# Kernel tuning notes

Hardware: AMD Instinct MI355X
Metric: run time of the kernel (lower is better)

## Reference

```python
import jax, jax.numpy as jnp
import numpy as np

PROCESSING_STEPS = 3


def setup_inputs() -> dict:
    key = jax.random.key(0)
    ks = jax.random.split(key, 8)
    B, N, d = 1024, 128, 128
    y = jax.random.normal(ks[0], (B, N, d), dtype=jnp.float32)
    lengths = jax.random.randint(ks[1], (B,), 1, N + 1, dtype=jnp.int32)
    s = 0.05
    W_ih = jax.random.normal(ks[2], (4 * d, 2 * d), dtype=jnp.float32) * s
    W_hh = jax.random.normal(ks[3], (4 * d, d), dtype=jnp.float32) * s
    b_ih = jax.random.normal(ks[4], (4 * d,), dtype=jnp.float32) * s
    b_hh = jax.random.normal(ks[5], (4 * d,), dtype=jnp.float32) * s
    W_m = jax.random.normal(ks[6], (1, 2 * d), dtype=jnp.float32) * s
    b_m = jax.random.normal(ks[7], (1,), dtype=jnp.float32) * s
    mean = jnp.zeros((1,), jnp.float32)
    stddev = jnp.ones((1,), jnp.float32)
    return {"y": y, "lengths": lengths, "W_ih": W_ih, "W_hh": W_hh,
            "b_ih": b_ih, "b_hh": b_hh, "W_m": W_m, "b_m": b_m,
            "mean": mean, "stddev": stddev}


def reference(y, lengths, W_ih, W_hh, b_ih, b_hh, W_m, b_m, mean, stddev):
    # y: [B, N, d] padded atomwise representation; lengths: valid atoms per molecule
    B, N, d = y.shape
    mask = jnp.arange(N)[None, :] < lengths[:, None]          # [B, N]
    maskf = mask.astype(y.dtype)[..., None]                    # [B, N, 1]
    neg_inf = jnp.finfo(y.dtype).min

    q_star = jnp.zeros((B, 2 * d), y.dtype)
    h = jnp.zeros((B, d), y.dtype)
    c = jnp.zeros((B, d), y.dtype)

    def step(carry, _):
        q_star, h, c = carry
        # single-layer LSTM cell (PyTorch gate order i, f, g, o)
        gates = q_star @ W_ih.T + b_ih + h @ W_hh.T + b_hh     # [B, 4d]
        i, f, g, o = jnp.split(gates, 4, axis=-1)
        c2 = jax.nn.sigmoid(f) * c + jax.nn.sigmoid(i) * jnp.tanh(g)
        h2 = jax.nn.sigmoid(o) * jnp.tanh(c2)
        q = h2                                                  # [B, d]
        # attention: gather q per atom, segment softmax, scatter_add
        e = jnp.einsum('bnd,bd->bn', y, q)                      # [B, N]
        e = jnp.where(mask, e, neg_inf)
        a = jax.nn.softmax(e, axis=-1)[..., None] * maskf       # [B, N, 1]
        r = jnp.sum(a * y, axis=1)                              # [B, d]
        return (jnp.concatenate([q, r], axis=-1), h2, c2), None

    (q_star, h, c), _ = jax.lax.scan(step, (q_star, h, c), None,
                                     length=PROCESSING_STEPS)
    out = q_star @ W_m.T + b_m                                  # [B, 1]
    return out * stddev + mean
```

## Files before the change

### kernel.cpp

```cpp
#include <hip/hip_runtime.h>
#include <math.h>

#define BB 1024
#define NN 128
#define DD 128
#define GG 512

__device__ __forceinline__ float sigmoidf_(float x) { return 1.0f / (1.0f + expf(-x)); }

__global__ __launch_bounds__(256) void k_prep(
    const float* __restrict__ W_ih, const float* __restrict__ W_hh,
    const float* __restrict__ b_ih, const float* __restrict__ b_hh,
    float* __restrict__ Wc, float* __restrict__ biasv, float* __restrict__ gbase,
    float* __restrict__ h1, float* __restrict__ c1) {
  int b = blockIdx.x, t = threadIdx.x;
  if (b < 64) {
    int base = b * 1024;
    for (int i = t; i < 1024; i += 256) {
      int idx = base + i;
      int j = idx >> 7, d = idx & 127;
      Wc[idx] = W_ih[(j << 8) + d] + W_hh[idx];
    }
  } else {
    __shared__ float bv[GG];
    __shared__ float h1l[DD];
    for (int j = t; j < GG; j += 256) bv[j] = b_ih[j] + b_hh[j];
    __syncthreads();
    if (t < DD) {
      float cc = sigmoidf_(bv[t]) * tanhf(bv[256 + t]);
      float hh = sigmoidf_(bv[384 + t]) * tanhf(cc);
      h1l[t] = hh;
      if (b == 64) { c1[t] = cc; h1[t] = hh; }
    }
    if (b == 64) for (int j = t; j < GG; j += 256) biasv[j] = bv[j];
    __syncthreads();
    int j0 = (b - 64) * 128;
    if (t < 128) {
      int j = j0 + t;
      float acc = bv[j];
      const float* wi = W_ih + (j << 8);
      const float* wh = W_hh + (j << 7);
      #pragma unroll 8
      for (int d = 0; d < DD; ++d) acc = fmaf(wi[d] + wh[d], h1l[d], acc);
      gbase[j] = acc;
    }
  }
}

__global__ __launch_bounds__(256) void k_attn(
    const float* __restrict__ y, const int* __restrict__ lengths,
    const float* __restrict__ qsrc, int q_bcast,
    float* __restrict__ rN,
    const float* __restrict__ Wm, const float* __restrict__ bm,
    const float* __restrict__ mn, const float* __restrict__ sd,
    float* __restrict__ out, int is_final) {
  __shared__ float ql[DD];
  __shared__ float rp[4][DD];
  __shared__ float redm[4], reds[4], redf[4];

  int t = threadIdx.x, lane = t & 63, w = t >> 6;
  int sub = lane & 15, g = lane >> 4;
  int m = blockIdx.x;
  int len = lengths[m];
  const float* yb = y + (size_t)m * (NN * DD);
  int d0 = sub << 3;

  if (t < DD) ql[t] = q_bcast ? qsrc[t] : qsrc[m * DD + t];
  __syncthreads();

  float4 q0 = *(const float4*)&ql[d0];
  float4 q1 = *(const float4*)&ql[d0 + 4];

  float4 va[8], vb[8];
  float ee[8];
  int wbase = w << 2;

  #pragma unroll
  for (int it = 0; it < 8; ++it) {
    int nw = (it << 4) + wbase;
    if (nw < len) {
      int n = nw + g;
      int nc = (n < len) ? n : (len - 1);
      const float4* yr = (const float4*)(yb + nc * DD + d0);
      va[it] = yr[0];
      vb[it] = yr[1];
      float p = fmaf(va[it].x, q0.x, fmaf(va[it].y, q0.y,
                fmaf(va[it].z, q0.z, fmaf(va[it].w, q0.w,
                fmaf(vb[it].x, q1.x, fmaf(vb[it].y, q1.y,
                fmaf(vb[it].z, q1.z, vb[it].w * q1.w)))))));
      #pragma unroll
      for (int s = 1; s < 16; s <<= 1) p += __shfl_xor(p, s, 64);
      ee[it] = (n < len) ? p : -3.0e38f;
    } else {
      ee[it] = -3.0e38f;
    }
  }

  float mloc = ee[0];
  #pragma unroll
  for (int it = 1; it < 8; ++it) mloc = fmaxf(mloc, ee[it]);
  #pragma unroll
  for (int s = 1; s < 64; s <<= 1) mloc = fmaxf(mloc, __shfl_xor(mloc, s, 64));

  float a[8];
  float sl = 0.0f;
  #pragma unroll
  for (int it = 0; it < 8; ++it) { a[it] = expf(ee[it] - mloc); sl += a[it]; }
  #pragma unroll
  for (int s = 1; s < 64; s <<= 1) sl += __shfl_xor(sl, s, 64);
  if (lane == 0) { redm[w] = mloc; reds[w] = sl; }
  __syncthreads();

  float m0_ = redm[0], m1_ = redm[1], m2_ = redm[2], m3_ = redm[3];
  float mx = fmaxf(fmaxf(m0_, m1_), fmaxf(m2_, m3_));
  float Zraw = reds[0] * expf(m0_ - mx) + reds[1] * expf(m1_ - mx) +
               reds[2] * expf(m2_ - mx) + reds[3] * expf(m3_ - mx);
  float wscale = expf(mloc - mx) * (16.0f / Zraw);

  float4 r0 = {0.f, 0.f, 0.f, 0.f}, r1 = {0.f, 0.f, 0.f, 0.f};
  #pragma unroll
  for (int it = 0; it < 8; ++it) {
    int nw = (it << 4) + wbase;
    if (nw < len) {
      float av = a[it];
      r0.x = fmaf(av, va[it].x, r0.x); r0.y = fmaf(av, va[it].y, r0.y);
      r0.z = fmaf(av, va[it].z, r0.z); r0.w = fmaf(av, va[it].w, r0.w);
      r1.x = fmaf(av, vb[it].x, r1.x); r1.y = fmaf(av, vb[it].y, r1.y);
      r1.z = fmaf(av, vb[it].z, r1.z); r1.w = fmaf(av, vb[it].w, r1.w);
    }
  }
  r0.x *= wscale; r0.y *= wscale; r0.z *= wscale; r0.w *= wscale;
  r1.x *= wscale; r1.y *= wscale; r1.z *= wscale; r1.w *= wscale;

  #pragma unroll
  for (int s = 16; s < 64; s <<= 1) {
    r0.x += __shfl_xor(r0.x, s, 64); r0.y += __shfl_xor(r0.y, s, 64);
    r0.z += __shfl_xor(r0.z, s, 64); r0.w += __shfl_xor(r0.w, s, 64);
    r1.x += __shfl_xor(r1.x, s, 64); r1.y += __shfl_xor(r1.y, s, 64);
    r1.z += __shfl_xor(r1.z, s, 64); r1.w += __shfl_xor(r1.w, s, 64);
  }
  if (g == 0) {
    *(float4*)&rp[w][d0] = r0;
    *(float4*)&rp[w][d0 + 4] = r1;
  }
  __syncthreads();

  float r_ = 0.0f;
  if (t < DD) {
    r_ = rp[0][t] + rp[1][t] + rp[2][t] + rp[3][t];
    if (!is_final) rN[m * DD + t] = r_;
  }
  if (is_final) {
    float part = (t < DD) ? (Wm[t] * ql[t] + Wm[DD + t] * r_) : 0.0f;
    #pragma unroll
    for (int s = 1; s < 64; s <<= 1) part += __shfl_xor(part, s, 64);
    if (lane == 0) redf[w] = part;
    __syncthreads();
    if (t == 0) out[m] = (redf[0] + redf[1] + redf[2] + redf[3] + bm[0]) * sd[0] + mn[0];
  }
}

__global__ __launch_bounds__(512) void k_lstm(
    const float* __restrict__ W_ih, const float* __restrict__ Wc,
    const float* __restrict__ gb,
    const float* __restrict__ h_inN,
    const float* __restrict__ c_in, int c_bcast,
    const float* __restrict__ rNin,
    float* __restrict__ h_outN, float* __restrict__ c_outT) {
  __shared__ float xl[64 * 129];
  __shared__ float ht[64 * 9];
  int t = threadIdx.x;
  int ml = t & 63, wid = t >> 6;
  int m0 = blockIdx.x << 6;
  int m = m0 + ml;
  int jb = __builtin_amdgcn_readfirstlane((blockIdx.y << 3) + wid);

  float ai = gb[jb], af = gb[DD + jb], ag = gb[2 * DD + jb], ao = gb[3 * DD + jb];

  if (h_inN) {
    #pragma unroll
    for (int k = 0; k < 16; ++k) {
      int i = (k << 9) + t;
      int mm = i >> 7, dd = i & 127;
      xl[mm * 129 + dd] = h_inN[(m0 + mm) * DD + dd];
    }
    __syncthreads();
    const float* w0 = Wc + jb * DD;
    const float* w1 = Wc + (128 + jb) * DD;
    const float* w2 = Wc + (256 + jb) * DD;
    const float* w3 = Wc + (384 + jb) * DD;
    #pragma unroll 8
    for (int d = 0; d < DD; ++d) {
      float xd = xl[ml * 129 + d];
      ai = fmaf(w0[d], xd, ai); af = fmaf(w1[d], xd, af);
      ag = fmaf(w2[d], xd, ag); ao = fmaf(w3[d], xd, ao);
    }
    __syncthreads();
  }

  #pragma unroll
  for (int k = 0; k < 16; ++k) {
    int i = (k << 9) + t;
    int mm = i >> 7, dd = i & 127;
    xl[mm * 129 + dd] = rNin[(m0 + mm) * DD + dd];
  }
  __syncthreads();
  {
    const float* w0 = W_ih + jb * 256 + 128;
    const float* w1 = W_ih + (128 + jb) * 256 + 128;
    const float* w2 = W_ih + (256 + jb) * 256 + 128;
    const float* w3 = W_ih + (384 + jb) * 256 + 128;
    #pragma unroll 8
    for (int d = 0; d < DD; ++d) {
      float xd = xl[ml * 129 + d];
      ai = fmaf(w0[d], xd, ai); af = fmaf(w1[d], xd, af);
      ag = fmaf(w2[d], xd, ag); ao = fmaf(w3[d], xd, ao);
    }
  }

  float cin = c_bcast ? c_in[jb] : c_in[jb * BB + m];
  float cc = fmaf(sigmoidf_(af), cin, sigmoidf_(ai) * tanhf(ag));
  float hh = sigmoidf_(ao) * tanhf(cc);
  ht[ml * 9 + wid] = hh;
  if (c_outT) c_outT[jb * BB + m] = cc;
  __syncthreads();
  {
    int jj = t & 7, mm = t >> 3;
    h_outN[(m0 + mm) * DD + (blockIdx.y << 3) + jj] = ht[mm * 9 + jj];
  }
}

extern "C" void kernel_launch(void* const* d_in, const int* in_sizes, int n_in,
                              void* d_out, int out_size, void* d_ws, size_t ws_size,
                              hipStream_t stream) {
  const float* y    = (const float*)d_in[0];
  const int*   len  = (const int*)  d_in[1];
  const float* W_ih = (const float*)d_in[2];
  const float* W_hh = (const float*)d_in[3];
  const float* b_ih = (const float*)d_in[4];
  const float* b_hh = (const float*)d_in[5];
  const float* W_m  = (const float*)d_in[6];
  const float* b_m  = (const float*)d_in[7];
  const float* mean = (const float*)d_in[8];
  const float* sd   = (const float*)d_in[9];
  float* out = (float*)d_out;

  float* ws = (float*)d_ws;
  float* Wc    = ws;
  float* biasv = ws + 65536;
  float* gbase = ws + 66048;
  float* h1    = ws + 66560;
  float* c1    = ws + 66688;
  float* rN    = ws + 66816;
  float* h2N   = ws + 197888;
  float* c2T   = ws + 328960;
  float* h3N   = ws + 460032;

  k_prep<<<68, 256, 0, stream>>>(W_ih, W_hh, b_ih, b_hh, Wc, biasv, gbase, h1, c1);

  k_attn<<<BB, 256, 0, stream>>>(y, len, h1, 1, rN, W_m, b_m, mean, sd, nullptr, 0);
  k_lstm<<<dim3(16, 16), 512, 0, stream>>>(W_ih, Wc, gbase, nullptr, c1, 1, rN, h2N, c2T);
  k_attn<<<BB, 256, 0, stream>>>(y, len, h2N, 0, rN, W_m, b_m, mean, sd, nullptr, 0);
  k_lstm<<<dim3(16, 16), 512, 0, stream>>>(W_ih, Wc, biasv, h2N, c2T, 0, rN, h3N, nullptr);
  k_attn<<<BB, 256, 0, stream>>>(y, len, h3N, 0, nullptr, W_m, b_m, mean, sd, out, 1);
}
```

Baseline: 63.62 us.

## Fold prep kernel into attention and LSTM kernels, pair molecules per block

Removes the separate k_prep launch. The first attention pass now computes the initial h from the biases inline, and the first LSTM step builds the combined W_ih+W_hh matrix and the base gates in-kernel. The attention kernel now handles two molecules per 512-thread block, pairing m with 1023-m to balance variable lengths, and issues all y loads before the dot products to raise memory-level parallelism. The cost is redundant bias and weight work repeated in every LSTM block, plus extra registers from loading all rows unconditionally, including clamped rows past the valid length.

```diff
diff --git a/kernel.cpp b/kernel.cpp
--- a/kernel.cpp
+++ b/kernel.cpp
@@ -4,86 +4,63 @@
 #define BB 1024
 #define NN 128
 #define DD 128
-#define GG 512
 
 __device__ __forceinline__ float sigmoidf_(float x) { return 1.0f / (1.0f + expf(-x)); }
 
-__global__ __launch_bounds__(256) void k_prep(
-    const float* __restrict__ W_ih, const float* __restrict__ W_hh,
+__global__ __launch_bounds__(512) void k_attn(
+    const float* __restrict__ y, const int* __restrict__ lengths,
+    const float* __restrict__ qsrc,
     const float* __restrict__ b_ih, const float* __restrict__ b_hh,
-    float* __restrict__ Wc, float* __restrict__ biasv, float* __restrict__ gbase,
-    float* __restrict__ h1, float* __restrict__ c1) {
-  int b = blockIdx.x, t = threadIdx.x;
-  if (b < 64) {
-    int base = b * 1024;
-    for (int i = t; i < 1024; i += 256) {
-      int idx = base + i;
-      int j = idx >> 7, d = idx & 127;
-      Wc[idx] = W_ih[(j << 8) + d] + W_hh[idx];
-    }
-  } else {
-    __shared__ float bv[GG];
-    __shared__ float h1l[DD];
-    for (int j = t; j < GG; j += 256) bv[j] = b_ih[j] + b_hh[j];
-    __syncthreads();
-    if (t < DD) {
-      float cc = sigmoidf_(bv[t]) * tanhf(bv[256 + t]);
-      float hh = sigmoidf_(bv[384 + t]) * tanhf(cc);
-      h1l[t] = hh;
-      if (b == 64) { c1[t] = cc; h1[t] = hh; }
-    }
-    if (b == 64) for (int j = t; j < GG; j += 256) biasv[j] = bv[j];
-    __syncthreads();
-    int j0 = (b - 64) * 128;
-    if (t < 128) {
-      int j = j0 + t;
-      float acc = bv[j];
-      const float* wi = W_ih + (j << 8);
-      const float* wh = W_hh + (j << 7);
-      #pragma unroll 8
-      for (int d = 0; d < DD; ++d) acc = fmaf(wi[d] + wh[d], h1l[d], acc);
-      gbase[j] = acc;
-    }
-  }
-}
-
-__global__ __launch_bounds__(256) void k_attn(
-    const float* __restrict__ y, const int* __restrict__ lengths,
-    const float* __restrict__ qsrc, int q_bcast,
     float* __restrict__ rN,
     const float* __restrict__ Wm, const float* __restrict__ bm,
     const float* __restrict__ mn, const float* __restrict__ sd,
     float* __restrict__ out, int is_final) {
-  __shared__ float ql[DD];
-  __shared__ float rp[4][DD];
-  __shared__ float redm[4], reds[4], redf[4];
+  __shared__ float ql[2][DD];
+  __shared__ float rp[2][4][DD];
+  __shared__ float redm[2][4], reds[2][4], redf[2][4];
 
   int t = threadIdx.x, lane = t & 63, w = t >> 6;
+  int h = w >> 2, w4 = w & 3;
   int sub = lane & 15, g = lane >> 4;
-  int m = blockIdx.x;
+  int m = h ? (1023 - (int)blockIdx.x) : (int)blockIdx.x;
   int len = lengths[m];
   const float* yb = y + (size_t)m * (NN * DD);
   int d0 = sub << 3;
-
-  if (t < DD) ql[t] = q_bcast ? qsrc[t] : qsrc[m * DD + t];
-  __syncthreads();
-
-  float4 q0 = *(const float4*)&ql[d0];
-  float4 q1 = *(const float4*)&ql[d0 + 4];
+  int th = t & 255;
+
+  if (th < DD) {
+    if (qsrc) {
+      ql[h][th] = qsrc[m * DD + th];
+    } else {
+      float bv0 = b_ih[th] + b_hh[th];
+      float bvg = b_ih[256 + th] + b_hh[256 + th];
+      float bvo = b_ih[384 + th] + b_hh[384 + th];
+      float cc = sigmoidf_(bv0) * tanhf(bvg);
+      ql[h][th] = sigmoidf_(bvo) * tanhf(cc);
+    }
+  }
+  __syncthreads();
+
+  float4 q0 = *(const float4*)&ql[h][d0];
+  float4 q1 = *(const float4*)&ql[h][d0 + 4];
 
   float4 va[8], vb[8];
+  int wbase = w4 << 2;
+  #pragma unroll
+  for (int it = 0; it < 8; ++it) {
+    int n = (it << 4) + wbase + g;
+    int nc = (n < len) ? n : (len - 1);
+    const float4* yr = (const float4*)(yb + nc * DD + d0);
+    va[it] = yr[0];
+    vb[it] = yr[1];
+  }
+
   float ee[8];
-  int wbase = w << 2;
-
   #pragma unroll
   for (int it = 0; it < 8; ++it) {
     int nw = (it << 4) + wbase;
     if (nw < len) {
       int n = nw + g;
-      int nc = (n < len) ? n : (len - 1);
-      const float4* yr = (const float4*)(yb + nc * DD + d0);
-      va[it] = yr[0];
-      vb[it] = yr[1];
       float p = fmaf(va[it].x, q0.x, fmaf(va[it].y, q0.y,
                 fmaf(va[it].z, q0.z, fmaf(va[it].w, q0.w,
                 fmaf(vb[it].x, q1.x, fmaf(vb[it].y, q1.y,
@@ -108,13 +85,13 @@
   for (int it = 0; it < 8; ++it) { a[it] = expf(ee[it] - mloc); sl += a[it]; }
   #pragma unroll
   for (int s = 1; s < 64; s <<= 1) sl += __shfl_xor(sl, s, 64);
-  if (lane == 0) { redm[w] = mloc; reds[w] = sl; }
-  __syncthreads();
-
-  float m0_ = redm[0], m1_ = redm[1], m2_ = redm[2], m3_ = redm[3];
+  if (lane == 0) { redm[h][w4] = mloc; reds[h][w4] = sl; }
+  __syncthreads();
+
+  float m0_ = redm[h][0], m1_ = redm[h][1], m2_ = redm[h][2], m3_ = redm[h][3];
   float mx = fmaxf(fmaxf(m0_, m1_), fmaxf(m2_, m3_));
-  float Zraw = reds[0] * expf(m0_ - mx) + reds[1] * expf(m1_ - mx) +
-               reds[2] * expf(m2_ - mx) + reds[3] * expf(m3_ - mx);
+  float Zraw = reds[h][0] * expf(m0_ - mx) + reds[h][1] * expf(m1_ - mx) +
+               reds[h][2] * expf(m2_ - mx) + reds[h][3] * expf(m3_ - mx);
   float wscale = expf(mloc - mx) * (16.0f / Zraw);
 
   float4 r0 = {0.f, 0.f, 0.f, 0.f}, r1 = {0.f, 0.f, 0.f, 0.f};
@@ -140,44 +117,79 @@
     r1.z += __shfl_xor(r1.z, s, 64); r1.w += __shfl_xor(r1.w, s, 64);
   }
   if (g == 0) {
-    *(float4*)&rp[w][d0] = r0;
-    *(float4*)&rp[w][d0 + 4] = r1;
+    *(float4*)&rp[h][w4][d0] = r0;
+    *(float4*)&rp[h][w4][d0 + 4] = r1;
   }
   __syncthreads();
 
   float r_ = 0.0f;
-  if (t < DD) {
-    r_ = rp[0][t] + rp[1][t] + rp[2][t] + rp[3][t];
-    if (!is_final) rN[m * DD + t] = r_;
+  if (th < DD) {
+    r_ = rp[h][0][th] + rp[h][1][th] + rp[h][2][th] + rp[h][3][th];
+    if (!is_final) rN[m * DD + th] = r_;
   }
   if (is_final) {
-    float part = (t < DD) ? (Wm[t] * ql[t] + Wm[DD + t] * r_) : 0.0f;
+    float part = (th < DD) ? (Wm[th] * ql[h][th] + Wm[DD + th] * r_) : 0.0f;
     #pragma unroll
     for (int s = 1; s < 64; s <<= 1) part += __shfl_xor(part, s, 64);
-    if (lane == 0) redf[w] = part;
-    __syncthreads();
-    if (t == 0) out[m] = (redf[0] + redf[1] + redf[2] + redf[3] + bm[0]) * sd[0] + mn[0];
+    if (lane == 0) redf[h][w4] = part;
+    __syncthreads();
+    if (th == 0)
+      out[m] = (redf[h][0] + redf[h][1] + redf[h][2] + redf[h][3] + bm[0]) * sd[0] + mn[0];
   }
 }
 
 __global__ __launch_bounds__(512) void k_lstm(
-    const float* __restrict__ W_ih, const float* __restrict__ Wc,
-    const float* __restrict__ gb,
+    const float* __restrict__ W_ih, const float* __restrict__ W_hh,
+    const float* __restrict__ b_ih, const float* __restrict__ b_hh,
+    float* __restrict__ Wc,
     const float* __restrict__ h_inN,
-    const float* __restrict__ c_in, int c_bcast,
+    const float* __restrict__ cT,
     const float* __restrict__ rNin,
-    float* __restrict__ h_outN, float* __restrict__ c_outT) {
+    float* __restrict__ h_outN, float* __restrict__ c_outT, int step) {
   __shared__ float xl[64 * 129];
+  __shared__ float h1l[DD];
   __shared__ float ht[64 * 9];
-  int t = threadIdx.x;
-  int ml = t & 63, wid = t >> 6;
-  int m0 = blockIdx.x << 6;
-  int m = m0 + ml;
-  int jb = __builtin_amdgcn_readfirstlane((blockIdx.y << 3) + wid);
-
-  float ai = gb[jb], af = gb[DD + jb], ag = gb[2 * DD + jb], ao = gb[3 * DD + jb];
-
-  if (h_inN) {
+  int t = threadIdx.x, lane = t & 63, wid = t >> 6;
+  int m0 = (int)blockIdx.x << 6, m = m0 + lane;
+  int jb = __builtin_amdgcn_readfirstlane(((int)blockIdx.y << 3) + wid);
+
+  float ai, af, ag, ao, cin;
+
+  if (step == 1) {
+    if (t < DD) {
+      float bv0 = b_ih[t] + b_hh[t];
+      float bvg = b_ih[256 + t] + b_hh[256 + t];
+      float bvo = b_ih[384 + t] + b_hh[384 + t];
+      float cc = sigmoidf_(bv0) * tanhf(bvg);
+      h1l[t] = sigmoidf_(bvo) * tanhf(cc);
+    }
+    __syncthreads();
+    int d = lane << 1;
+    float acc4[4];
+    #pragma unroll
+    for (int gi = 0; gi < 4; ++gi) {
+      int j = jb + (gi << 7);
+      float2 wih = *(const float2*)&W_ih[j * 256 + d];
+      float2 whh = *(const float2*)&W_hh[(j << 7) + d];
+      float s0 = wih.x + whh.x, s1 = wih.y + whh.y;
+      if (blockIdx.x == 0) {
+        Wc[(j << 7) + d] = s0;
+        Wc[(j << 7) + d + 1] = s1;
+      }
+      float part = fmaf(s0, h1l[d], s1 * h1l[d + 1]);
+      #pragma unroll
+      for (int s = 1; s < 64; s <<= 1) part += __shfl_xor(part, s, 64);
+      acc4[gi] = part + b_ih[j] + b_hh[j];
+    }
+    ai = acc4[0]; af = acc4[1]; ag = acc4[2]; ao = acc4[3];
+    cin = sigmoidf_(b_ih[jb] + b_hh[jb]) *
+          tanhf(b_ih[256 + jb] + b_hh[256 + jb]);
+  } else {
+    ai = b_ih[jb] + b_hh[jb];
+    af = b_ih[128 + jb] + b_hh[128 + jb];
+    ag = b_ih[256 + jb] + b_hh[256 + jb];
+    ao = b_ih[384 + jb] + b_hh[384 + jb];
+    cin = cT[(jb << 10) + m];
     #pragma unroll
     for (int k = 0; k < 16; ++k) {
       int i = (k << 9) + t;
@@ -185,15 +197,15 @@
       xl[mm * 129 + dd] = h_inN[(m0 + mm) * DD + dd];
     }
     __syncthreads();
-    const float* w0 = Wc + jb * DD;
-    const float* w1 = Wc + (128 + jb) * DD;
-    const float* w2 = Wc + (256 + jb) * DD;
-    const float* w3 = Wc + (384 + jb) * DD;
+    const float* w0 = Wc + (jb << 7);
+    const float* w1 = Wc + ((128 + jb) << 7);
+    const float* w2 = Wc + ((256 + jb) << 7);
+    const float* w3 = Wc + ((384 + jb) << 7);
     #pragma unroll 8
-    for (int d = 0; d < DD; ++d) {
-      float xd = xl[ml * 129 + d];
-      ai = fmaf(w0[d], xd, ai); af = fmaf(w1[d], xd, af);
-      ag = fmaf(w2[d], xd, ag); ao = fmaf(w3[d], xd, ao);
+    for (int dd = 0; dd < DD; ++dd) {
+      float xd = xl[lane * 129 + dd];
+      ai = fmaf(w0[dd], xd, ai); af = fmaf(w1[dd], xd, af);
+      ag = fmaf(w2[dd], xd, ag); ao = fmaf(w3[dd], xd, ao);
     }
     __syncthreads();
   }
@@ -211,22 +223,21 @@
     const float* w2 = W_ih + (256 + jb) * 256 + 128;
     const float* w3 = W_ih + (384 + jb) * 256 + 128;
     #pragma unroll 8
-    for (int d = 0; d < DD; ++d) {
-      float xd = xl[ml * 129 + d];
-      ai = fmaf(w0[d], xd, ai); af = fmaf(w1[d], xd, af);
-      ag = fmaf(w2[d], xd, ag); ao = fmaf(w3[d], xd, ao);
-    }
-  }
-
-  float cin = c_bcast ? c_in[jb] : c_in[jb * BB + m];
+    for (int dd = 0; dd < DD; ++dd) {
+      float xd = xl[lane * 129 + dd];
+      ai = fmaf(w0[dd], xd, ai); af = fmaf(w1[dd], xd, af);
+      ag = fmaf(w2[dd], xd, ag); ao = fmaf(w3[dd], xd, ao);
+    }
+  }
+
   float cc = fmaf(sigmoidf_(af), cin, sigmoidf_(ai) * tanhf(ag));
   float hh = sigmoidf_(ao) * tanhf(cc);
-  ht[ml * 9 + wid] = hh;
-  if (c_outT) c_outT[jb * BB + m] = cc;
+  ht[lane * 9 + wid] = hh;
+  if (c_outT) c_outT[(jb << 10) + m] = cc;
   __syncthreads();
   {
     int jj = t & 7, mm = t >> 3;
-    h_outN[(m0 + mm) * DD + (blockIdx.y << 3) + jj] = ht[mm * 9 + jj];
+    h_outN[(m0 + mm) * DD + ((int)blockIdx.y << 3) + jj] = ht[mm * 9 + jj];
   }
 }
 
@@ -246,21 +257,20 @@
   float* out = (float*)d_out;
 
   float* ws = (float*)d_ws;
-  float* Wc    = ws;
-  float* biasv = ws + 65536;
-  float* gbase = ws + 66048;
-  float* h1    = ws + 66560;
-  float* c1    = ws + 66688;
-  float* rN    = ws + 66816;
-  float* h2N   = ws + 197888;
-  float* c2T   = ws + 328960;
-  float* h3N   = ws + 460032;
-
-  k_prep<<<68, 256, 0, stream>>>(W_ih, W_hh, b_ih, b_hh, Wc, biasv, gbase, h1, c1);
-
-  k_attn<<<BB, 256, 0, stream>>>(y, len, h1, 1, rN, W_m, b_m, mean, sd, nullptr, 0);
-  k_lstm<<<dim3(16, 16), 512, 0, stream>>>(W_ih, Wc, gbase, nullptr, c1, 1, rN, h2N, c2T);
-  k_attn<<<BB, 256, 0, stream>>>(y, len, h2N, 0, rN, W_m, b_m, mean, sd, nullptr, 0);
-  k_lstm<<<dim3(16, 16), 512, 0, stream>>>(W_ih, Wc, biasv, h2N, c2T, 0, rN, h3N, nullptr);
-  k_attn<<<BB, 256, 0, stream>>>(y, len, h3N, 0, nullptr, W_m, b_m, mean, sd, out, 1);
+  float* Wc  = ws;
+  float* rN  = ws + 65536;
+  float* h2N = ws + 196608;
+  float* c2T = ws + 327680;
+  float* h3N = ws + 458752;
+
+  k_attn<<<512, 512, 0, stream>>>(y, len, nullptr, b_ih, b_hh, rN,
+                                  W_m, b_m, mean, sd, nullptr, 0);
+  k_lstm<<<dim3(16, 16), 512, 0, stream>>>(W_ih, W_hh, b_ih, b_hh, Wc,
+                                           nullptr, nullptr, rN, h2N, c2T, 1);
+  k_attn<<<512, 512, 0, stream>>>(y, len, h2N, b_ih, b_hh, rN,
+                                  W_m, b_m, mean, sd, nullptr, 0);
+  k_lstm<<<dim3(16, 16), 512, 0, stream>>>(W_ih, W_hh, b_ih, b_hh, Wc,
+                                           h2N, c2T, rN, h3N, nullptr, 2);
+  k_attn<<<512, 512, 0, stream>>>(y, len, h3N, b_ih, b_hh, nullptr,
+                                  W_m, b_m, mean, sd, out, 1);
 }
```

New measurement: 61.35 us. -3.6%, faster.

## Fuse all attention and LSTM steps into one persistent per-molecule-pair kernel

Applied to the files above, without the earlier changes.

Replaces the three attention launches and two LSTM launches with a single kernel in which each 512-thread block handles two molecules (one per half). Each molecule's y rows are kept in registers and reused across all three processing steps, and the LSTM gates are computed in-block from a combined weight matrix. This removes repeated reads of y from global memory, the intermediate h/r/c round-trips and four kernel launches. In exchange every block re-reads the full 512x256 weight matrix from L2/global, and register pressure under launch_bounds(512,4) may limit occupancy.

```diff
diff --git a/kernel.cpp b/kernel.cpp
--- a/kernel.cpp
+++ b/kernel.cpp
@@ -4,230 +4,247 @@
 #define BB 1024
 #define NN 128
 #define DD 128
-#define GG 512
 
 __device__ __forceinline__ float sigmoidf_(float x) { return 1.0f / (1.0f + expf(-x)); }
 
-__global__ __launch_bounds__(256) void k_prep(
+__global__ __launch_bounds__(256) void k_prep2(
     const float* __restrict__ W_ih, const float* __restrict__ W_hh,
     const float* __restrict__ b_ih, const float* __restrict__ b_hh,
-    float* __restrict__ Wc, float* __restrict__ biasv, float* __restrict__ gbase,
-    float* __restrict__ h1, float* __restrict__ c1) {
+    float* __restrict__ Wfull, float* __restrict__ gbase) {
   int b = blockIdx.x, t = threadIdx.x;
   if (b < 64) {
-    int base = b * 1024;
-    for (int i = t; i < 1024; i += 256) {
+    int base = b * 2048;
+    for (int i = t; i < 2048; i += 256) {
       int idx = base + i;
-      int j = idx >> 7, d = idx & 127;
-      Wc[idx] = W_ih[(j << 8) + d] + W_hh[idx];
+      int j = idx >> 8, d = idx & 255;
+      float v = W_ih[(j << 8) + d];
+      if (d < 128) v += W_hh[(j << 7) + d];
+      Wfull[idx] = v;
     }
   } else {
-    __shared__ float bv[GG];
     __shared__ float h1l[DD];
-    for (int j = t; j < GG; j += 256) bv[j] = b_ih[j] + b_hh[j];
-    __syncthreads();
     if (t < DD) {
-      float cc = sigmoidf_(bv[t]) * tanhf(bv[256 + t]);
-      float hh = sigmoidf_(bv[384 + t]) * tanhf(cc);
-      h1l[t] = hh;
-      if (b == 64) { c1[t] = cc; h1[t] = hh; }
-    }
-    if (b == 64) for (int j = t; j < GG; j += 256) biasv[j] = bv[j];
+      float bi = b_ih[t] + b_hh[t];
+      float bg = b_ih[256 + t] + b_hh[256 + t];
+      float bo = b_ih[384 + t] + b_hh[384 + t];
+      float cc = sigmoidf_(bi) * tanhf(bg);
+      h1l[t] = sigmoidf_(bo) * tanhf(cc);
+    }
     __syncthreads();
     int j0 = (b - 64) * 128;
     if (t < 128) {
       int j = j0 + t;
-      float acc = bv[j];
-      const float* wi = W_ih + (j << 8);
-      const float* wh = W_hh + (j << 7);
+      float acc = b_ih[j] + b_hh[j];
       #pragma unroll 8
-      for (int d = 0; d < DD; ++d) acc = fmaf(wi[d] + wh[d], h1l[d], acc);
+      for (int d = 0; d < DD; ++d)
+        acc = fmaf(W_ih[(j << 8) + d] + W_hh[(j << 7) + d], h1l[d], acc);
       gbase[j] = acc;
     }
   }
 }
 
-__global__ __launch_bounds__(256) void k_attn(
+struct SMX {
+  float ql[2][DD];
+  float c1l[DD];
+  float rp[2][4][DD];
+  float xcat[2][256];
+  float g2[2][512];
+  float c2l[2][DD];
+  float redm[2][4], reds[2][4], redf[2][4];
+};
+
+__global__ __launch_bounds__(512, 4) void k_fused(
     const float* __restrict__ y, const int* __restrict__ lengths,
-    const float* __restrict__ qsrc, int q_bcast,
-    float* __restrict__ rN,
+    const float* __restrict__ Wfull, const float* __restrict__ gbase,
+    const float* __restrict__ b_ih, const float* __restrict__ b_hh,
     const float* __restrict__ Wm, const float* __restrict__ bm,
     const float* __restrict__ mn, const float* __restrict__ sd,
-    float* __restrict__ out, int is_final) {
-  __shared__ float ql[DD];
-  __shared__ float rp[4][DD];
-  __shared__ float redm[4], reds[4], redf[4];
-
-  int t = threadIdx.x, lane = t & 63, w = t >> 6;
-  int sub = lane & 15, g = lane >> 4;
-  int m = blockIdx.x;
-  int len = lengths[m];
+    float* __restrict__ out) {
+  __shared__ SMX s;
+  const int t = threadIdx.x;
+  const int lane = t & 63;
+  const int h = t >> 8;
+  const int th = t & 255;
+  const int w4 = (t >> 6) & 3;
+  const int sub = lane & 15, g = lane >> 4;
+  const int d0 = sub << 3;
+  const int wbase = w4 << 2;
+  const int m = h ? (1023 - (int)blockIdx.x) : (int)blockIdx.x;
+  const int len = lengths[m];
   const float* yb = y + (size_t)m * (NN * DD);
-  int d0 = sub << 3;
-
-  if (t < DD) ql[t] = q_bcast ? qsrc[t] : qsrc[m * DD + t];
-  __syncthreads();
-
-  float4 q0 = *(const float4*)&ql[d0];
-  float4 q1 = *(const float4*)&ql[d0 + 4];
+
+  if (th < DD) {
+    float bi = b_ih[th] + b_hh[th];
+    float bg = b_ih[256 + th] + b_hh[256 + th];
+    float bo = b_ih[384 + th] + b_hh[384 + th];
+    float cc = sigmoidf_(bi) * tanhf(bg);
+    s.ql[h][th] = sigmoidf_(bo) * tanhf(cc);
+    if (h == 0) s.c1l[th] = cc;
+  }
 
   float4 va[8], vb[8];
-  float ee[8];
-  int wbase = w << 2;
-
   #pragma unroll
   for (int it = 0; it < 8; ++it) {
-    int nw = (it << 4) + wbase;
-    if (nw < len) {
-      int n = nw + g;
-      int nc = (n < len) ? n : (len - 1);
-      const float4* yr = (const float4*)(yb + nc * DD + d0);
-      va[it] = yr[0];
-      vb[it] = yr[1];
-      float p = fmaf(va[it].x, q0.x, fmaf(va[it].y, q0.y,
-                fmaf(va[it].z, q0.z, fmaf(va[it].w, q0.w,
-                fmaf(vb[it].x, q1.x, fmaf(vb[it].y, q1.y,
-                fmaf(vb[it].z, q1.z, vb[it].w * q1.w)))))));
+    int n = (it << 4) + wbase + g;
+    int nc = (n < len) ? n : (len - 1);
+    const float4* yr = (const float4*)(yb + nc * DD + d0);
+    va[it] = yr[0];
+    vb[it] = yr[1];
+  }
+  __syncthreads();
+
+  auto attn = [&](float* rdst, bool is_final) {
+    float4 q0 = *(const float4*)&s.ql[h][d0];
+    float4 q1 = *(const float4*)&s.ql[h][d0 + 4];
+    float ee[8];
+    #pragma unroll
+    for (int it = 0; it < 8; ++it) {
+      int nw = (it << 4) + wbase;
+      if (nw < len) {
+        int n = nw + g;
+        float p = fmaf(va[it].x, q0.x, fmaf(va[it].y, q0.y,
+                  fmaf(va[it].z, q0.z, fmaf(va[it].w, q0.w,
+                  fmaf(vb[it].x, q1.x, fmaf(vb[it].y, q1.y,
+                  fmaf(vb[it].z, q1.z, vb[it].w * q1.w)))))));
+        #pragma unroll
+        for (int sh = 1; sh < 16; sh <<= 1) p += __shfl_xor(p, sh, 64);
+        ee[it] = (n < len) ? p : -3.0e38f;
+      } else {
+        ee[it] = -3.0e38f;
+      }
+    }
+    float mloc = ee[0];
+    #pragma unroll
+    for (int it = 1; it < 8; ++it) mloc = fmaxf(mloc, ee[it]);
+    #pragma unroll
+    for (int sh = 1; sh < 64; sh <<= 1) mloc = fmaxf(mloc, __shfl_xor(mloc, sh, 64));
+    float a[8], sl = 0.0f;
+    #pragma unroll
+    for (int it = 0; it < 8; ++it) { a[it] = expf(ee[it] - mloc); sl += a[it]; }
+    #pragma unroll
+    for (int sh = 1; sh < 64; sh <<= 1) sl += __shfl_xor(sl, sh, 64);
+    if (lane == 0) { s.redm[h][w4] = mloc; s.reds[h][w4] = sl; }
+    __syncthreads();
+    float m0_ = s.redm[h][0], m1_ = s.redm[h][1], m2_ = s.redm[h][2], m3_ = s.redm[h][3];
+    float mx = fmaxf(fmaxf(m0_, m1_), fmaxf(m2_, m3_));
+    float Zraw = s.reds[h][0] * expf(m0_ - mx) + s.reds[h][1] * expf(m1_ - mx) +
+                 s.reds[h][2] * expf(m2_ - mx) + s.reds[h][3] * expf(m3_ - mx);
+    float wscale = expf(mloc - mx) * (16.0f / Zraw);
+
+    float4 r0 = {0.f, 0.f, 0.f, 0.f}, r1 = {0.f, 0.f, 0.f, 0.f};
+    #pragma unroll
+    for (int it = 0; it < 8; ++it) {
+      int nw = (it << 4) + wbase;
+      if (nw < len) {
+        float av = a[it];
+        r0.x = fmaf(av, va[it].x, r0.x); r0.y = fmaf(av, va[it].y, r0.y);
+        r0.z = fmaf(av, va[it].z, r0.z); r0.w = fmaf(av, va[it].w, r0.w);
+        r1.x = fmaf(av, vb[it].x, r1.x); r1.y = fmaf(av, vb[it].y, r1.y);
+        r1.z = fmaf(av, vb[it].z, r1.z); r1.w = fmaf(av, vb[it].w, r1.w);
+      }
+    }
+    r0.x *= wscale; r0.y *= wscale; r0.z *= wscale; r0.w *= wscale;
+    r1.x *= wscale; r1.y *= wscale; r1.z *= wscale; r1.w *= wscale;
+    #pragma unroll
+    for (int sh = 16; sh < 64; sh <<= 1) {
+      r0.x += __shfl_xor(r0.x, sh, 64); r0.y += __shfl_xor(r0.y, sh, 64);
+      r0.z += __shfl_xor(r0.z, sh, 64); r0.w += __shfl_xor(r0.w, sh, 64);
+      r1.x += __shfl_xor(r1.x, sh, 64); r1.y += __shfl_xor(r1.y, sh, 64);
+      r1.z += __shfl_xor(r1.z, sh, 64); r1.w += __shfl_xor(r1.w, sh, 64);
+    }
+    if (g == 0) {
+      *(float4*)&s.rp[h][w4][d0] = r0;
+      *(float4*)&s.rp[h][w4][d0 + 4] = r1;
+    }
+    __syncthreads();
+    float r_ = 0.0f;
+    if (th < DD) {
+      r_ = s.rp[h][0][th] + s.rp[h][1][th] + s.rp[h][2][th] + s.rp[h][3][th];
+      if (!is_final) rdst[th] = r_;
+    }
+    if (is_final) {
+      float part = (th < DD) ? (Wm[th] * s.ql[h][th] + Wm[DD + th] * r_) : 0.0f;
       #pragma unroll
-      for (int s = 1; s < 16; s <<= 1) p += __shfl_xor(p, s, 64);
-      ee[it] = (n < len) ? p : -3.0e38f;
+      for (int sh = 1; sh < 64; sh <<= 1) part += __shfl_xor(part, sh, 64);
+      if (lane == 0) s.redf[h][w4] = part;
+      __syncthreads();
+      if (th == 0)
+        out[m] = (s.redf[h][0] + s.redf[h][1] + s.redf[h][2] + s.redf[h][3] + bm[0])
+                 * sd[0] + mn[0];
     } else {
-      ee[it] = -3.0e38f;
-    }
-  }
-
-  float mloc = ee[0];
-  #pragma unroll
-  for (int it = 1; it < 8; ++it) mloc = fmaxf(mloc, ee[it]);
-  #pragma unroll
-  for (int s = 1; s < 64; s <<= 1) mloc = fmaxf(mloc, __shfl_xor(mloc, s, 64));
-
-  float a[8];
-  float sl = 0.0f;
-  #pragma unroll
-  for (int it = 0; it < 8; ++it) { a[it] = expf(ee[it] - mloc); sl += a[it]; }
-  #pragma unroll
-  for (int s = 1; s < 64; s <<= 1) sl += __shfl_xor(sl, s, 64);
-  if (lane == 0) { redm[w] = mloc; reds[w] = sl; }
-  __syncthreads();
-
-  float m0_ = redm[0], m1_ = redm[1], m2_ = redm[2], m3_ = redm[3];
-  float mx = fmaxf(fmaxf(m0_, m1_), fmaxf(m2_, m3_));
-  float Zraw = reds[0] * expf(m0_ - mx) + reds[1] * expf(m1_ - mx) +
-               reds[2] * expf(m2_ - mx) + reds[3] * expf(m3_ - mx);
-  float wscale = expf(mloc - mx) * (16.0f / Zraw);
-
-  float4 r0 = {0.f, 0.f, 0.f, 0.f}, r1 = {0.f, 0.f, 0.f, 0.f};
-  #pragma unroll
-  for (int it = 0; it < 8; ++it) {
-    int nw = (it << 4) + wbase;
-    if (nw < len) {
-      float av = a[it];
-      r0.x = fmaf(av, va[it].x, r0.x); r0.y = fmaf(av, va[it].y, r0.y);
-      r0.z = fmaf(av, va[it].z, r0.z); r0.w = fmaf(av, va[it].w, r0.w);
-      r1.x = fmaf(av, vb[it].x, r1.x); r1.y = fmaf(av, vb[it].y, r1.y);
-      r1.z = fmaf(av, vb[it].z, r1.z); r1.w = fmaf(av, vb[it].w, r1.w);
-    }
-  }
-  r0.x *= wscale; r0.y *= wscale; r0.z *= wscale; r0.w *= wscale;
-  r1.x *= wscale; r1.y *= wscale; r1.z *= wscale; r1.w *= wscale;
-
-  #pragma unroll
-  for (int s = 16; s < 64; s <<= 1) {
-    r0.x += __shfl_xor(r0.x, s, 64); r0.y += __shfl_xor(r0.y, s, 64);
-    r0.z += __shfl_xor(r0.z, s, 64); r0.w += __shfl_xor(r0.w, s, 64);
-    r1.x += __shfl_xor(r1.x, s, 64); r1.y += __shfl_xor(r1.y, s, 64);
-    r1.z += __shfl_xor(r1.z, s, 64); r1.w += __shfl_xor(r1.w, s, 64);
-  }
-  if (g == 0) {
-    *(float4*)&rp[w][d0] = r0;
-    *(float4*)&rp[w][d0 + 4] = r1;
-  }
-  __syncthreads();
-
-  float r_ = 0.0f;
-  if (t < DD) {
-    r_ = rp[0][t] + rp[1][t] + rp[2][t] + rp[3][t];
-    if (!is_final) rN[m * DD + t] = r_;
-  }
-  if (is_final) {
-    float part = (t < DD) ? (Wm[t] * ql[t] + Wm[DD + t] * r_) : 0.0f;
-    #pragma unroll
-    for (int s = 1; s < 64; s <<= 1) part += __shfl_xor(part, s, 64);
-    if (lane == 0) redf[w] = part;
-    __syncthreads();
-    if (t == 0) out[m] = (redf[0] + redf[1] + redf[2] + redf[3] + bm[0]) * sd[0] + mn[0];
-  }
-}
-
-__global__ __launch_bounds__(512) void k_lstm(
-    const float* __restrict__ W_ih, const float* __restrict__ Wc,
-    const float* __restrict__ gb,
-    const float* __restrict__ h_inN,
-    const float* __restrict__ c_in, int c_bcast,
-    const float* __restrict__ rNin,
-    float* __restrict__ h_outN, float* __restrict__ c_outT) {
-  __shared__ float xl[64 * 129];
-  __shared__ float ht[64 * 9];
-  int t = threadIdx.x;
-  int ml = t & 63, wid = t >> 6;
-  int m0 = blockIdx.x << 6;
-  int m = m0 + ml;
-  int jb = __builtin_amdgcn_readfirstlane((blockIdx.y << 3) + wid);
-
-  float ai = gb[jb], af = gb[DD + jb], ag = gb[2 * DD + jb], ao = gb[3 * DD + jb];
-
-  if (h_inN) {
-    #pragma unroll
-    for (int k = 0; k < 16; ++k) {
-      int i = (k << 9) + t;
-      int mm = i >> 7, dd = i & 127;
-      xl[mm * 129 + dd] = h_inN[(m0 + mm) * DD + dd];
-    }
-    __syncthreads();
-    const float* w0 = Wc + jb * DD;
-    const float* w1 = Wc + (128 + jb) * DD;
-    const float* w2 = Wc + (256 + jb) * DD;
-    const float* w3 = Wc + (384 + jb) * DD;
-    #pragma unroll 8
-    for (int d = 0; d < DD; ++d) {
-      float xd = xl[ml * 129 + d];
-      ai = fmaf(w0[d], xd, ai); af = fmaf(w1[d], xd, af);
-      ag = fmaf(w2[d], xd, ag); ao = fmaf(w3[d], xd, ao);
-    }
-    __syncthreads();
-  }
-
-  #pragma unroll
-  for (int k = 0; k < 16; ++k) {
-    int i = (k << 9) + t;
-    int mm = i >> 7, dd = i & 127;
-    xl[mm * 129 + dd] = rNin[(m0 + mm) * DD + dd];
-  }
-  __syncthreads();
+      __syncthreads();
+    }
+  };
+
+  attn(&s.xcat[h][128], false);
+
   {
-    const float* w0 = W_ih + jb * 256 + 128;
-    const float* w1 = W_ih + (128 + jb) * 256 + 128;
-    const float* w2 = W_ih + (256 + jb) * 256 + 128;
-    const float* w3 = W_ih + (384 + jb) * 256 + 128;
-    #pragma unroll 8
-    for (int d = 0; d < DD; ++d) {
-      float xd = xl[ml * 129 + d];
-      ai = fmaf(w0[d], xd, ai); af = fmaf(w1[d], xd, af);
-      ag = fmaf(w2[d], xd, ag); ao = fmaf(w3[d], xd, ao);
-    }
-  }
-
-  float cin = c_bcast ? c_in[jb] : c_in[jb * BB + m];
-  float cc = fmaf(sigmoidf_(af), cin, sigmoidf_(ai) * tanhf(ag));
-  float hh = sigmoidf_(ao) * tanhf(cc);
-  ht[ml * 9 + wid] = hh;
-  if (c_outT) c_outT[jb * BB + m] = cc;
-  __syncthreads();
+    int j = t;
+    float bA = gbase[j];
+    float aA0 = bA, aA1 = 0.f, aB0 = bA, aB1 = 0.f;
+    const float4* wr = (const float4*)(Wfull + (j << 8) + 128);
+    const float4* xA = (const float4*)&s.xcat[0][128];
+    const float4* xB = (const float4*)&s.xcat[1][128];
+    #pragma unroll 2
+    for (int k = 0; k < 32; k += 2) {
+      float4 w0 = wr[k], w1 = wr[k + 1];
+      float4 a0 = xA[k], a1 = xA[k + 1];
+      float4 b0 = xB[k], b1 = xB[k + 1];
+      aA0 = fmaf(w0.x, a0.x, fmaf(w0.y, a0.y, fmaf(w0.z, a0.z, fmaf(w0.w, a0.w, aA0))));
+      aA1 = fmaf(w1.x, a1.x, fmaf(w1.y, a1.y, fmaf(w1.z, a1.z, fmaf(w1.w, a1.w, aA1))));
+      aB0 = fmaf(w0.x, b0.x, fmaf(w0.y, b0.y, fmaf(w0.z, b0.z, fmaf(w0.w, b0.w, aB0))));
+      aB1 = fmaf(w1.x, b1.x, fmaf(w1.y, b1.y, fmaf(w1.z, b1.z, fmaf(w1.w, b1.w, aB1))));
+    }
+    s.g2[0][j] = aA0 + aA1;
+    s.g2[1][j] = aB0 + aB1;
+  }
+  __syncthreads();
+  if (t < 256) {
+    int mol = t >> 7, u = t & 127;
+    float I = s.g2[mol][u], F = s.g2[mol][128 + u];
+    float G = s.g2[mol][256 + u], O = s.g2[mol][384 + u];
+    float cc = fmaf(sigmoidf_(F), s.c1l[u], sigmoidf_(I) * tanhf(G));
+    float hh = sigmoidf_(O) * tanhf(cc);
+    s.c2l[mol][u] = cc;
+    s.xcat[mol][u] = hh;
+    s.ql[mol][u] = hh;
+  }
+  __syncthreads();
+
+  attn(&s.xcat[h][128], false);
+
   {
-    int jj = t & 7, mm = t >> 3;
-    h_outN[(m0 + mm) * DD + (blockIdx.y << 3) + jj] = ht[mm * 9 + jj];
-  }
+    int j = t;
+    float bA = b_ih[j] + b_hh[j];
+    float aA0 = bA, aA1 = 0.f, aB0 = bA, aB1 = 0.f;
+    const float4* wr = (const float4*)(Wfull + (j << 8));
+    const float4* xA = (const float4*)&s.xcat[0][0];
+    const float4* xB = (const float4*)&s.xcat[1][0];
+    #pragma unroll 2
+    for (int k = 0; k < 64; k += 2) {
+      float4 w0 = wr[k], w1 = wr[k + 1];
+      float4 a0 = xA[k], a1 = xA[k + 1];
+      float4 b0 = xB[k], b1 = xB[k + 1];
+      aA0 = fmaf(w0.x, a0.x, fmaf(w0.y, a0.y, fmaf(w0.z, a0.z, fmaf(w0.w, a0.w, aA0))));
+      aA1 = fmaf(w1.x, a1.x, fmaf(w1.y, a1.y, fmaf(w1.z, a1.z, fmaf(w1.w, a1.w, aA1))));
+      aB0 = fmaf(w0.x, b0.x, fmaf(w0.y, b0.y, fmaf(w0.z, b0.z, fmaf(w0.w, b0.w, aB0))));
+      aB1 = fmaf(w1.x, b1.x, fmaf(w1.y, b1.y, fmaf(w1.z, b1.z, fmaf(w1.w, b1.w, aB1))));
+    }
+    s.g2[0][j] = aA0 + aA1;
+    s.g2[1][j] = aB0 + aB1;
+  }
+  __syncthreads();
+  if (t < 256) {
+    int mol = t >> 7, u = t & 127;
+    float I = s.g2[mol][u], F = s.g2[mol][128 + u];
+    float G = s.g2[mol][256 + u], O = s.g2[mol][384 + u];
+    float cc = fmaf(sigmoidf_(F), s.c2l[mol][u], sigmoidf_(I) * tanhf(G));
+    float hh = sigmoidf_(O) * tanhf(cc);
+    s.ql[mol][u] = hh;
+  }
+  __syncthreads();
+
+  attn(nullptr, true);
 }
 
 extern "C" void kernel_launch(void* const* d_in, const int* in_sizes, int n_in,
@@ -245,22 +262,11 @@
   const float* sd   = (const float*)d_in[9];
   float* out = (float*)d_out;
 
-  float* ws = (float*)d_ws;
-  float* Wc    = ws;
-  float* biasv = ws + 65536;
-  float* gbase = ws + 66048;
-  float* h1    = ws + 66560;
-  float* c1    = ws + 66688;
-  float* rN    = ws + 66816;
-  float* h2N   = ws + 197888;
-  float* c2T   = ws + 328960;
-  float* h3N   = ws + 460032;
-
-  k_prep<<<68, 256, 0, stream>>>(W_ih, W_hh, b_ih, b_hh, Wc, biasv, gbase, h1, c1);
-
-  k_attn<<<BB, 256, 0, stream>>>(y, len, h1, 1, rN, W_m, b_m, mean, sd, nullptr, 0);
-  k_lstm<<<dim3(16, 16), 512, 0, stream>>>(W_ih, Wc, gbase, nullptr, c1, 1, rN, h2N, c2T);
-  k_attn<<<BB, 256, 0, stream>>>(y, len, h2N, 0, rN, W_m, b_m, mean, sd, nullptr, 0);
-  k_lstm<<<dim3(16, 16), 512, 0, stream>>>(W_ih, Wc, biasv, h2N, c2T, 0, rN, h3N, nullptr);
-  k_attn<<<BB, 256, 0, stream>>>(y, len, h3N, 0, nullptr, W_m, b_m, mean, sd, out, 1);
+  float* ws    = (float*)d_ws;
+  float* Wfull = ws;
+  float* gbase = ws + 131072;
+
+  k_prep2<<<68, 256, 0, stream>>>(W_ih, W_hh, b_ih, b_hh, Wfull, gbase);
+  k_fused<<<512, 512, 0, stream>>>(y, len, Wfull, gbase, b_ih, b_hh,
+                                   W_m, b_m, mean, sd, out);
 }
```

Measured after the change: 73.06 us. 1.15x slower.
